# Kernel tuning notes

Hardware: AMD Instinct MI355X
Metric: run time of the kernel (lower is better)

Reference implementation:

```python
import jax, jax.numpy as jnp
import numpy as np

N_NODES = 50000
N_EDGES = 800000
IN_DIM = 256
N_HEADS = 4
D_HEAD = 32  # out_dim // num_heads = 128 // 4
NEG_SLOPE = 0.01  # F.leaky_relu default


def setup_inputs() -> dict:
    key = jax.random.key(0)
    k1, k2, k3, k4, k5 = jax.random.split(key, 5)
    h = jax.random.normal(k1, (N_NODES, IN_DIM), dtype=jnp.float32)
    # per-head projection weights, xavier-ish scale
    fc_w = jax.random.normal(k2, (N_HEADS, IN_DIM, D_HEAD), dtype=jnp.float32) * (1.0 / np.sqrt(IN_DIM))
    attn_w = jax.random.normal(k3, (N_HEADS, 2 * D_HEAD), dtype=jnp.float32) * (1.0 / np.sqrt(2 * D_HEAD))
    src = jax.random.randint(k4, (N_EDGES,), 0, N_NODES, dtype=jnp.int32)
    dst = jax.random.randint(k5, (N_EDGES,), 0, N_NODES, dtype=jnp.int32)
    return {"h": h, "fc_w": fc_w, "attn_w": attn_w, "src": src, "dst": dst,
            "num_bits": 8, "num_grad_bits": 8}


def reference(h, fc_w, attn_w, src, dst, num_bits, num_grad_bits):
    # num_bits/num_grad_bits only used in quant_agg branch (disabled in source)
    N = h.shape[0]
    # per-head linear projection: [N, H, dh]
    z = jnp.einsum('ni,hid->nhd', h, fc_w)
    z_src = z[src]  # [E, H, dh]
    z_dst = z[dst]  # [E, H, dh]
    # edge attention score: attn_fc(cat[z_src, z_dst]) -> split weight halves
    a_src, a_dst = attn_w[:, :D_HEAD], attn_w[:, D_HEAD:]
    e = (jnp.einsum('ehd,hd->eh', z_src, a_src)
         + jnp.einsum('ehd,hd->eh', z_dst, a_dst))  # [E, H]
    e = jnp.where(e >= 0, e, NEG_SLOPE * e)  # leaky_relu
    # segment softmax over incoming edges per destination node
    m = jax.ops.segment_max(e, dst, num_segments=N)  # [N, H]
    ex = jnp.exp(e - m[dst])
    denom = jax.ops.segment_sum(ex, dst, num_segments=N)  # [N, H]
    alpha = ex / denom[dst]  # [E, H]
    # scatter weighted aggregation
    out = jax.ops.segment_sum(alpha[:, :, None] * z_src, dst, num_segments=N)  # [N, H, dh]
    # merge='cat' over heads
    return out.reshape(N, N_HEADS * D_HEAD)
```

## Files before the change

### kernel.cpp

```cpp
#include <hip/hip_runtime.h>
#include <hip/hip_bf16.h>
#include <math.h>

#define N_HEADS 4
#define D_HEAD 32
#define IN_DIM 256
#define OUT_DIM (N_HEADS * D_HEAD)
#define NEG_SLOPE 0.01f

#define BSHIFT 7
#define BUCK_NODES 128
#define CAP 4096
#define CHUNK 8192

typedef __attribute__((ext_vector_type(8))) short bf16x8;
typedef __attribute__((ext_vector_type(4))) float f32x4;
typedef __attribute__((ext_vector_type(2))) float f32x2;

static __device__ __forceinline__ unsigned short f2bf(float x)
{
    unsigned int u = __float_as_uint(x);
    u = u + 0x7FFFu + ((u >> 16) & 1u);
    return (unsigned short)(u >> 16);
}

static __device__ __forceinline__ unsigned int pack_bf2(float a, float b)
{
    union { __hip_bfloat162 b2; unsigned int u; } r;
    r.b2 = __float22bfloat162_rn(make_float2(a, b));
    return r.u;
}

static __device__ __forceinline__ f32x2 bfpair(unsigned int u)
{
    f32x2 r;
    r.x = __uint_as_float(u << 16);
    r.y = __uint_as_float(u & 0xFFFF0000u);
    return r;
}

__global__ void setup_kernel(const float* __restrict__ fc_w,
                             unsigned short* __restrict__ wl,
                             int* __restrict__ bucket_fill, int nbuck)
{
    int o = blockIdx.x * blockDim.x + threadIdx.x;
    if (o < nbuck) bucket_fill[o] = 0;
    if (o >= 32768) return;
    int j  = o & 7;
    int l  = (o >> 3) & 63;
    int kf = (o >> 9) & 7;
    int cf = (o >> 12) & 7;
    int k   = kf * 32 + (l >> 4) * 8 + j;
    int col = cf * 16 + (l & 15);
    int hh = col >> 5, d = col & 31;
    wl[o] = f2bf(fc_w[hh * 8192 + k * 32 + d]);
}

__global__ __launch_bounds__(512, 4) void fused_kernel(
    const float* __restrict__ h, const unsigned short* __restrict__ wl,
    const float* __restrict__ attn_w,
    unsigned int* __restrict__ zb,
    float* __restrict__ s_src, float* __restrict__ s_dst,
    int n_nodes,
    const int* __restrict__ src, const int* __restrict__ dst,
    int* __restrict__ bucket_fill, unsigned int* __restrict__ scratch,
    int n_edges, int nbuck, int nA)
{
    __shared__ __align__(16) char smem[65536];
    const int t = threadIdx.x;

    if (blockIdx.x < nA) {
        int* bhist = (int*)smem;
        int* boff  = (int*)(smem + 2048);
        int* goff  = (int*)(smem + 4096);
        int* bcur  = (int*)(smem + 6144);
        int* stmp  = (int*)(smem + 8192);
        unsigned int* lpair = (unsigned int*)(smem + 10240);

        const int e0 = blockIdx.x * CHUNK;
        const int n  = min(CHUNK, n_edges - e0);

        bhist[t] = 0;
        __syncthreads();

        for (int i = t; i < n; i += 512) {
            atomicAdd(&bhist[dst[e0 + i] >> BSHIFT], 1);
        }
        __syncthreads();

        int v = bhist[t];
        int x = v;
        stmp[t] = x;
        __syncthreads();
        for (int off = 1; off < 512; off <<= 1) {
            int y = (t >= off) ? stmp[t - off] : 0;
            __syncthreads();
            x += y;
            stmp[t] = x;
            __syncthreads();
        }
        int excl = x - v;
        boff[t] = excl;
        bcur[t] = excl;

        goff[t] = (v > 0 && t < nbuck) ? (t * CAP + atomicAdd(&bucket_fill[t], v)) : 0;
        __syncthreads();

        for (int i = t; i < n; i += 512) {
            int d  = dst[e0 + i];
            int sv = src[e0 + i];
            int p  = atomicAdd(&bcur[d >> BSHIFT], 1);
            lpair[p] = ((unsigned int)d << 16) | (unsigned int)sv;
        }
        __syncthreads();

        const int lim = nbuck * CAP - 1;
        for (int i = t; i < n; i += 512) {
            unsigned int u = lpair[i];
            int b = (int)(u >> 16) >> BSHIFT;
            int addr = goff[b] + (i - boff[b]);
            scratch[min(addr, lim)] = u;
        }
        return;
    }

    unsigned short* wls = (unsigned short*)smem;

    #pragma unroll
    for (int it = 0; it < 8; ++it) {
        ((uint4*)wls)[t + it * 512] = ((const uint4*)wl)[t + it * 512];
    }
    __syncthreads();

    const int w  = t >> 6;
    const int l  = t & 63;
    const int g  = l >> 4;
    const int ln = l & 15;
    const int m0 = (blockIdx.x - nA) * 128 + w * 16;

    const int arow = min(m0 + ln, n_nodes - 1);
    const float4* hrow = (const float4*)(h + (size_t)arow * IN_DIM);

    f32x4 acc[8];
    #pragma unroll
    for (int cf = 0; cf < 8; ++cf) acc[cf] = (f32x4){0.f, 0.f, 0.f, 0.f};

    #pragma unroll
    for (int kf = 0; kf < 8; ++kf) {
        float4 alo = hrow[kf * 8 + g * 2];
        float4 ahi = hrow[kf * 8 + g * 2 + 1];
        union { unsigned int u[4]; bf16x8 v; } fa;
        fa.u[0] = pack_bf2(alo.x, alo.y);
        fa.u[1] = pack_bf2(alo.z, alo.w);
        fa.u[2] = pack_bf2(ahi.x, ahi.y);
        fa.u[3] = pack_bf2(ahi.z, ahi.w);

        #pragma unroll
        for (int cf = 0; cf < 8; ++cf) {
            bf16x8 fb = *(const bf16x8*)&wls[((cf * 8 + kf) * 64 + l) * 8];
            acc[cf] = __builtin_amdgcn_mfma_f32_16x16x32_bf16(fa.v, fb, acc[cf], 0, 0, 0);
        }
    }

    float aw_s[8], aw_d[8];
    #pragma unroll
    for (int cf = 0; cf < 8; ++cf) {
        int col = cf * 16 + ln;
        int hh = col >> 5, d = col & 31;
        aw_s[cf] = attn_w[hh * 64 + d];
        aw_d[cf] = attn_w[hh * 64 + 32 + d];
    }

    #pragma unroll
    for (int r = 0; r < 4; ++r) {
        const int row = m0 + 4 * g + r;
        const bool ok = (row < n_nodes);

        float vs0 = acc[0][r] * aw_s[0] + acc[1][r] * aw_s[1];
        float vs1 = acc[2][r] * aw_s[2] + acc[3][r] * aw_s[3];
        float vs2 = acc[4][r] * aw_s[4] + acc[5][r] * aw_s[5];
        float vs3 = acc[6][r] * aw_s[6] + acc[7][r] * aw_s[7];
        float vd0 = acc[0][r] * aw_d[0] + acc[1][r] * aw_d[1];
        float vd1 = acc[2][r] * aw_d[2] + acc[3][r] * aw_d[3];
        float vd2 = acc[4][r] * aw_d[4] + acc[5][r] * aw_d[5];
        float vd3 = acc[6][r] * aw_d[6] + acc[7][r] * aw_d[7];
        #pragma unroll
        for (int mk = 1; mk < 16; mk <<= 1) {
            vs0 += __shfl_xor(vs0, mk); vs1 += __shfl_xor(vs1, mk);
            vs2 += __shfl_xor(vs2, mk); vs3 += __shfl_xor(vs3, mk);
            vd0 += __shfl_xor(vd0, mk); vd1 += __shfl_xor(vd1, mk);
            vd2 += __shfl_xor(vd2, mk); vd3 += __shfl_xor(vd3, mk);
        }
        float sel_s = (ln == 0) ? vs0 : (ln == 1) ? vs1 : (ln == 2) ? vs2 : vs3;
        float sel_d = ((ln & 3) == 0) ? vd0 : ((ln & 3) == 1) ? vd1 : ((ln & 3) == 2) ? vd2 : vd3;
        if (ok && ln < 4)              s_src[row * N_HEADS + ln]       = sel_s;
        if (ok && ln >= 4 && ln < 8)   s_dst[row * N_HEADS + (ln & 3)] = sel_d;

        #pragma unroll
        for (int cf = 0; cf < 8; ++cf) {
            float v = acc[cf][r];
            float o = __shfl_xor(v, 1);
            if (!(ln & 1) && ok) {
                zb[(size_t)row * 64 + cf * 8 + (ln >> 1)] = pack_bf2(v, o);
            }
        }
    }
}

__global__ __launch_bounds__(256) void bucketB_kernel(
    const unsigned int* __restrict__ scratch,
    const int* __restrict__ bucket_fill,
    int* __restrict__ row_start,
    int* __restrict__ sorted_src,
    int n_nodes, int nbuck, int n_edges)
{
    __shared__ int pref[512];
    __shared__ int lhist[128];
    __shared__ int lcur[128];
    __shared__ int stmp[256];
    __shared__ unsigned int ent[CAP];

    const int b = blockIdx.x;
    const int t = threadIdx.x;

    {
        int a0 = (2 * t     < nbuck) ? min(bucket_fill[2 * t],     CAP) : 0;
        int a1 = (2 * t + 1 < nbuck) ? min(bucket_fill[2 * t + 1], CAP) : 0;
        int s = a0 + a1;
        int x = s;
        stmp[t] = x;
        __syncthreads();
        for (int off = 1; off < 256; off <<= 1) {
            int y = (t >= off) ? stmp[t - off] : 0;
            __syncthreads();
            x += y;
            stmp[t] = x;
            __syncthreads();
        }
        int excl = x - s;
        pref[2 * t]     = excl;
        pref[2 * t + 1] = excl + a0;
    }
    __syncthreads();

    const int cnt_b = min(bucket_fill[b], CAP);
    const int row0  = pref[b];
    const unsigned int* sb = scratch + (size_t)b * CAP;

    if (b == 0 && t == 0) row_start[n_nodes] = n_edges;

    if (t < 128) lhist[t] = 0;
    __syncthreads();

    for (int i = t; i < cnt_b; i += 256) {
        unsigned int u = sb[i];
        ent[i] = u;
        atomicAdd(&lhist[(u >> 16) & (BUCK_NODES - 1)], 1);
    }
    __syncthreads();

    int v = (t < 128) ? lhist[t] : 0;
    int x = v;
    stmp[t] = x;
    __syncthreads();
    for (int off = 1; off < 128; off <<= 1) {
        int y = (t >= off) ? stmp[t - off] : 0;
        __syncthreads();
        x += y;
        stmp[t] = x;
        __syncthreads();
    }
    if (t < 128) {
        int excl = x - v;
        lcur[t] = excl;
        int node = b * BUCK_NODES + t;
        if (node < n_nodes) row_start[node] = row0 + excl;
    }
    __syncthreads();

    for (int i = t; i < cnt_b; i += 256) {
        unsigned int u = ent[i];
        int dl = (u >> 16) & (BUCK_NODES - 1);
        int r = atomicAdd(&lcur[dl], 1);
        sorted_src[row0 + r] = (int)(u & 0xFFFFu);
    }
}

__global__ __launch_bounds__(256) void gather_kernel(
    const int* __restrict__ sorted_src, const int* __restrict__ row_start,
    const unsigned int* __restrict__ zb,
    const float* __restrict__ s_src, const float* __restrict__ s_dst,
    float* __restrict__ out, int n_nodes)
{
    int wave = (blockIdx.x * 256 + threadIdx.x) >> 6;
    int lane = threadIdx.x & 63;
    int half = lane >> 5;
    int node = wave * 2 + half;
    int g2   = (lane >> 4) & 1;
    int q    = lane & 15;
    int hh   = q >> 2;

    const bool valid = (node < n_nodes);
    const int nclamp = min(node, n_nodes - 1);
    const int b0 = row_start[nclamp];
    int deg = row_start[nclamp + 1] - b0;
    if (!valid) deg = 0;

    f32x2 acc2[4];
    #pragma unroll
    for (int i = 0; i < 4; ++i) acc2[i] = (f32x2){0.f, 0.f};
    float den = 0.0f;

    if (deg > 0) {
        const int* sp = sorted_src + b0;
        const float sdst = s_dst[nclamp * N_HEADS + hh];
        const int dm1 = deg - 1;

        for (int p = 0; p < deg; p += 8) {
            int i0 = p + g2, i1 = p + 2 + g2, i2 = p + 4 + g2, i3 = p + 6 + g2;
            int s0 = sp[min(i0, dm1)];
            int s1 = sp[min(i1, dm1)];
            int s2 = sp[min(i2, dm1)];
            int s3 = sp[min(i3, dm1)];

            float f0 = s_src[s0 * N_HEADS + hh];
            float f1 = s_src[s1 * N_HEADS + hh];
            float f2 = s_src[s2 * N_HEADS + hh];
            float f3 = s_src[s3 * N_HEADS + hh];
            uint4 u0 = *(const uint4*)&zb[(size_t)s0 * 64 + q * 4];
            uint4 u1 = *(const uint4*)&zb[(size_t)s1 * 64 + q * 4];
            uint4 u2 = *(const uint4*)&zb[(size_t)s2 * 64 + q * 4];
            uint4 u3 = *(const uint4*)&zb[(size_t)s3 * 64 + q * 4];

            float e0 = f0 + sdst; e0 = fmaxf(e0, NEG_SLOPE * e0);
            float e1 = f1 + sdst; e1 = fmaxf(e1, NEG_SLOPE * e1);
            float e2 = f2 + sdst; e2 = fmaxf(e2, NEG_SLOPE * e2);
            float e3 = f3 + sdst; e3 = fmaxf(e3, NEG_SLOPE * e3);
            float x0 = (i0 <= dm1) ? __expf(e0) : 0.0f;
            float x1 = (i1 <= dm1) ? __expf(e1) : 0.0f;
            float x2 = (i2 <= dm1) ? __expf(e2) : 0.0f;
            float x3 = (i3 <= dm1) ? __expf(e3) : 0.0f;
            den += (x0 + x1) + (x2 + x3);

            f32x2 xv;
            xv = (f32x2){x0, x0};
            acc2[0] += xv * bfpair(u0.x);
            acc2[1] += xv * bfpair(u0.y);
            acc2[2] += xv * bfpair(u0.z);
            acc2[3] += xv * bfpair(u0.w);
            xv = (f32x2){x1, x1};
            acc2[0] += xv * bfpair(u1.x);
            acc2[1] += xv * bfpair(u1.y);
            acc2[2] += xv * bfpair(u1.z);
            acc2[3] += xv * bfpair(u1.w);
            xv = (f32x2){x2, x2};
            acc2[0] += xv * bfpair(u2.x);
            acc2[1] += xv * bfpair(u2.y);
            acc2[2] += xv * bfpair(u2.z);
            acc2[3] += xv * bfpair(u2.w);
            xv = (f32x2){x3, x3};
            acc2[0] += xv * bfpair(u3.x);
            acc2[1] += xv * bfpair(u3.y);
            acc2[2] += xv * bfpair(u3.z);
            acc2[3] += xv * bfpair(u3.w);
        }
    }

    #pragma unroll
    for (int i = 0; i < 4; ++i) {
        acc2[i].x += __shfl_xor(acc2[i].x, 16);
        acc2[i].y += __shfl_xor(acc2[i].y, 16);
    }
    den += __shfl_xor(den, 16);

    if (g2 == 0 && valid) {
        float inv = (deg > 0) ? 1.0f / den : 0.0f;
        float4 v0 = make_float4(acc2[0].x * inv, acc2[0].y * inv, acc2[1].x * inv, acc2[1].y * inv);
        float4 v1 = make_float4(acc2[2].x * inv, acc2[2].y * inv, acc2[3].x * inv, acc2[3].y * inv);
        float4* op = (float4*)&out[(size_t)node * OUT_DIM + q * 8];
        op[0] = v0;
        op[1] = v1;
    }
}

extern "C" void kernel_launch(void* const* d_in, const int* in_sizes, int n_in,
                              void* d_out, int out_size, void* d_ws, size_t ws_size,
                              hipStream_t stream)
{
    const float* h      = (const float*)d_in[0];
    const float* fc_w   = (const float*)d_in[1];
    const float* attn_w = (const float*)d_in[2];
    const int*   src    = (const int*)d_in[3];
    const int*   dst    = (const int*)d_in[4];

    const int n_nodes = in_sizes[0] / IN_DIM;
    const int n_edges = in_sizes[3];
    const int nbuck   = (n_nodes + BUCK_NODES - 1) / BUCK_NODES;

    float* out = (float*)d_out;

    char* ws = (char*)d_ws;
    unsigned int* zb      = (unsigned int*)ws;
    float* s_src          = (float*)(zb + (size_t)n_nodes * 64);
    float* s_dst          = s_src + (size_t)n_nodes * N_HEADS;
    int*   row_start      = (int*)(s_dst + (size_t)n_nodes * N_HEADS);
    int*   bucket_fill    = row_start + n_nodes + 16;
    int*   sorted_src     = bucket_fill + nbuck + 17;
    unsigned int* scratch = (unsigned int*)(sorted_src + n_edges + 16);
    unsigned short* wl_g  = (unsigned short*)(scratch + (size_t)nbuck * CAP);

    const int nA = (n_edges + CHUNK - 1) / CHUNK;
    const int nG = (n_nodes + 127) / 128;

    setup_kernel<<<128, 256, 0, stream>>>(fc_w, wl_g, bucket_fill, nbuck);

    fused_kernel<<<nA + nG, 512, 0, stream>>>(
        h, wl_g, attn_w, zb, s_src, s_dst, n_nodes,
        src, dst, bucket_fill, scratch, n_edges, nbuck, nA);

    bucketB_kernel<<<nbuck, 256, 0, stream>>>(
        scratch, bucket_fill, row_start, sorted_src, n_nodes, nbuck, n_edges);

    {
        int waves = (n_nodes + 1) / 2;
        int blocks = (waves * 64 + 255) / 256;
        gather_kernel<<<blocks, 256, 0, stream>>>(
            sorted_src, row_start, zb, s_src, s_dst, out, n_nodes);
    }
}
```

Before: 70.84 us.

## Merge bucket-sort second pass into fused kernel with spin-wait completion counter

Folds the bucketB pass into the fused projection/bucketing kernel as extra trailing blocks. Phase-A blocks bump a global completion counter after a threadfence, and bucket blocks spin until every phase-A block has finished before running the prefix scan and local sort, now with 512 threads. This removes one kernel launch and lets the bucket sort overlap with the projection GEMM blocks. It depends on blocks being scheduled in index order to avoid deadlock, and spinning blocks hold CU slots while they wait.

```diff
diff --git a/kernel.cpp b/kernel.cpp
--- a/kernel.cpp
+++ b/kernel.cpp
@@ -44,7 +44,7 @@
                              int* __restrict__ bucket_fill, int nbuck)
 {
     int o = blockIdx.x * blockDim.x + threadIdx.x;
-    if (o < nbuck) bucket_fill[o] = 0;
+    if (o <= nbuck) bucket_fill[o] = 0;
     if (o >= 32768) return;
     int j  = o & 7;
     int l  = (o >> 3) & 63;
@@ -56,7 +56,7 @@
     wl[o] = f2bf(fc_w[hh * 8192 + k * 32 + d]);
 }
 
-__global__ __launch_bounds__(512, 4) void fused_kernel(
+__global__ __launch_bounds__(512, 4) void mega_kernel(
     const float* __restrict__ h, const unsigned short* __restrict__ wl,
     const float* __restrict__ attn_w,
     unsigned int* __restrict__ zb,
@@ -64,7 +64,8 @@
     int n_nodes,
     const int* __restrict__ src, const int* __restrict__ dst,
     int* __restrict__ bucket_fill, unsigned int* __restrict__ scratch,
-    int n_edges, int nbuck, int nA)
+    int* __restrict__ row_start, int* __restrict__ sorted_src,
+    int n_edges, int nbuck, int nA, int nG)
 {
     __shared__ __align__(16) char smem[65536];
     const int t = threadIdx.x;
@@ -121,168 +122,170 @@
             int addr = goff[b] + (i - boff[b]);
             scratch[min(addr, lim)] = u;
         }
+
+        __syncthreads();
+        __threadfence();
+        if (t == 0) atomicAdd(&bucket_fill[nbuck], 1);
         return;
     }
 
-    unsigned short* wls = (unsigned short*)smem;
-
-    #pragma unroll
-    for (int it = 0; it < 8; ++it) {
-        ((uint4*)wls)[t + it * 512] = ((const uint4*)wl)[t + it * 512];
-    }
-    __syncthreads();
-
-    const int w  = t >> 6;
-    const int l  = t & 63;
-    const int g  = l >> 4;
-    const int ln = l & 15;
-    const int m0 = (blockIdx.x - nA) * 128 + w * 16;
-
-    const int arow = min(m0 + ln, n_nodes - 1);
-    const float4* hrow = (const float4*)(h + (size_t)arow * IN_DIM);
-
-    f32x4 acc[8];
-    #pragma unroll
-    for (int cf = 0; cf < 8; ++cf) acc[cf] = (f32x4){0.f, 0.f, 0.f, 0.f};
-
-    #pragma unroll
-    for (int kf = 0; kf < 8; ++kf) {
-        float4 alo = hrow[kf * 8 + g * 2];
-        float4 ahi = hrow[kf * 8 + g * 2 + 1];
-        union { unsigned int u[4]; bf16x8 v; } fa;
-        fa.u[0] = pack_bf2(alo.x, alo.y);
-        fa.u[1] = pack_bf2(alo.z, alo.w);
-        fa.u[2] = pack_bf2(ahi.x, ahi.y);
-        fa.u[3] = pack_bf2(ahi.z, ahi.w);
-
+    if (blockIdx.x < nA + nG) {
+        unsigned short* wls = (unsigned short*)smem;
+
+        #pragma unroll
+        for (int it = 0; it < 8; ++it) {
+            ((uint4*)wls)[t + it * 512] = ((const uint4*)wl)[t + it * 512];
+        }
+        __syncthreads();
+
+        const int w  = t >> 6;
+        const int l  = t & 63;
+        const int g  = l >> 4;
+        const int ln = l & 15;
+        const int m0 = (blockIdx.x - nA) * 128 + w * 16;
+
+        const int arow = min(m0 + ln, n_nodes - 1);
+        const float4* hrow = (const float4*)(h + (size_t)arow * IN_DIM);
+
+        f32x4 acc[8];
+        #pragma unroll
+        for (int cf = 0; cf < 8; ++cf) acc[cf] = (f32x4){0.f, 0.f, 0.f, 0.f};
+
+        #pragma unroll
+        for (int kf = 0; kf < 8; ++kf) {
+            float4 alo = hrow[kf * 8 + g * 2];
+            float4 ahi = hrow[kf * 8 + g * 2 + 1];
+            union { unsigned int u[4]; bf16x8 v; } fa;
+            fa.u[0] = pack_bf2(alo.x, alo.y);
+            fa.u[1] = pack_bf2(alo.z, alo.w);
+            fa.u[2] = pack_bf2(ahi.x, ahi.y);
+            fa.u[3] = pack_bf2(ahi.z, ahi.w);
+
+            #pragma unroll
+            for (int cf = 0; cf < 8; ++cf) {
+                bf16x8 fb = *(const bf16x8*)&wls[((cf * 8 + kf) * 64 + l) * 8];
+                acc[cf] = __builtin_amdgcn_mfma_f32_16x16x32_bf16(fa.v, fb, acc[cf], 0, 0, 0);
+            }
+        }
+
+        float aw_s[8], aw_d[8];
         #pragma unroll
         for (int cf = 0; cf < 8; ++cf) {
-            bf16x8 fb = *(const bf16x8*)&wls[((cf * 8 + kf) * 64 + l) * 8];
-            acc[cf] = __builtin_amdgcn_mfma_f32_16x16x32_bf16(fa.v, fb, acc[cf], 0, 0, 0);
-        }
-    }
-
-    float aw_s[8], aw_d[8];
-    #pragma unroll
-    for (int cf = 0; cf < 8; ++cf) {
-        int col = cf * 16 + ln;
-        int hh = col >> 5, d = col & 31;
-        aw_s[cf] = attn_w[hh * 64 + d];
-        aw_d[cf] = attn_w[hh * 64 + 32 + d];
-    }
-
-    #pragma unroll
-    for (int r = 0; r < 4; ++r) {
-        const int row = m0 + 4 * g + r;
-        const bool ok = (row < n_nodes);
-
-        float vs0 = acc[0][r] * aw_s[0] + acc[1][r] * aw_s[1];
-        float vs1 = acc[2][r] * aw_s[2] + acc[3][r] * aw_s[3];
-        float vs2 = acc[4][r] * aw_s[4] + acc[5][r] * aw_s[5];
-        float vs3 = acc[6][r] * aw_s[6] + acc[7][r] * aw_s[7];
-        float vd0 = acc[0][r] * aw_d[0] + acc[1][r] * aw_d[1];
-        float vd1 = acc[2][r] * aw_d[2] + acc[3][r] * aw_d[3];
-        float vd2 = acc[4][r] * aw_d[4] + acc[5][r] * aw_d[5];
-        float vd3 = acc[6][r] * aw_d[6] + acc[7][r] * aw_d[7];
+            int col = cf * 16 + ln;
+            int hh = col >> 5, d = col & 31;
+            aw_s[cf] = attn_w[hh * 64 + d];
+            aw_d[cf] = attn_w[hh * 64 + 32 + d];
+        }
+
         #pragma unroll
-        for (int mk = 1; mk < 16; mk <<= 1) {
-            vs0 += __shfl_xor(vs0, mk); vs1 += __shfl_xor(vs1, mk);
-            vs2 += __shfl_xor(vs2, mk); vs3 += __shfl_xor(vs3, mk);
-            vd0 += __shfl_xor(vd0, mk); vd1 += __shfl_xor(vd1, mk);
-            vd2 += __shfl_xor(vd2, mk); vd3 += __shfl_xor(vd3, mk);
-        }
-        float sel_s = (ln == 0) ? vs0 : (ln == 1) ? vs1 : (ln == 2) ? vs2 : vs3;
-        float sel_d = ((ln & 3) == 0) ? vd0 : ((ln & 3) == 1) ? vd1 : ((ln & 3) == 2) ? vd2 : vd3;
-        if (ok && ln < 4)              s_src[row * N_HEADS + ln]       = sel_s;
-        if (ok && ln >= 4 && ln < 8)   s_dst[row * N_HEADS + (ln & 3)] = sel_d;
-
-        #pragma unroll
-        for (int cf = 0; cf < 8; ++cf) {
-            float v = acc[cf][r];
-            float o = __shfl_xor(v, 1);
-            if (!(ln & 1) && ok) {
-                zb[(size_t)row * 64 + cf * 8 + (ln >> 1)] = pack_bf2(v, o);
+        for (int r = 0; r < 4; ++r) {
+            const int row = m0 + 4 * g + r;
+            const bool ok = (row < n_nodes);
+
+            float vs0 = acc[0][r] * aw_s[0] + acc[1][r] * aw_s[1];
+            float vs1 = acc[2][r] * aw_s[2] + acc[3][r] * aw_s[3];
+            float vs2 = acc[4][r] * aw_s[4] + acc[5][r] * aw_s[5];
+            float vs3 = acc[6][r] * aw_s[6] + acc[7][r] * aw_s[7];
+            float vd0 = acc[0][r] * aw_d[0] + acc[1][r] * aw_d[1];
+            float vd1 = acc[2][r] * aw_d[2] + acc[3][r] * aw_d[3];
+            float vd2 = acc[4][r] * aw_d[4] + acc[5][r] * aw_d[5];
+            float vd3 = acc[6][r] * aw_d[6] + acc[7][r] * aw_d[7];
+            #pragma unroll
+            for (int mk = 1; mk < 16; mk <<= 1) {
+                vs0 += __shfl_xor(vs0, mk); vs1 += __shfl_xor(vs1, mk);
+                vs2 += __shfl_xor(vs2, mk); vs3 += __shfl_xor(vs3, mk);
+                vd0 += __shfl_xor(vd0, mk); vd1 += __shfl_xor(vd1, mk);
+                vd2 += __shfl_xor(vd2, mk); vd3 += __shfl_xor(vd3, mk);
             }
-        }
-    }
-}
-
-__global__ __launch_bounds__(256) void bucketB_kernel(
-    const unsigned int* __restrict__ scratch,
-    const int* __restrict__ bucket_fill,
-    int* __restrict__ row_start,
-    int* __restrict__ sorted_src,
-    int n_nodes, int nbuck, int n_edges)
-{
-    __shared__ int pref[512];
-    __shared__ int lhist[128];
-    __shared__ int lcur[128];
-    __shared__ int stmp[256];
-    __shared__ unsigned int ent[CAP];
-
-    const int b = blockIdx.x;
-    const int t = threadIdx.x;
+            float sel_s = (ln == 0) ? vs0 : (ln == 1) ? vs1 : (ln == 2) ? vs2 : vs3;
+            float sel_d = ((ln & 3) == 0) ? vd0 : ((ln & 3) == 1) ? vd1 : ((ln & 3) == 2) ? vd2 : vd3;
+            if (ok && ln < 4)              s_src[row * N_HEADS + ln]       = sel_s;
+            if (ok && ln >= 4 && ln < 8)   s_dst[row * N_HEADS + (ln & 3)] = sel_d;
+
+            #pragma unroll
+            for (int cf = 0; cf < 8; ++cf) {
+                float v = acc[cf][r];
+                float o = __shfl_xor(v, 1);
+                if (!(ln & 1) && ok) {
+                    zb[(size_t)row * 64 + cf * 8 + (ln >> 1)] = pack_bf2(v, o);
+                }
+            }
+        }
+        return;
+    }
 
     {
-        int a0 = (2 * t     < nbuck) ? min(bucket_fill[2 * t],     CAP) : 0;
-        int a1 = (2 * t + 1 < nbuck) ? min(bucket_fill[2 * t + 1], CAP) : 0;
-        int s = a0 + a1;
-        int x = s;
-        stmp[t] = x;
-        __syncthreads();
-        for (int off = 1; off < 256; off <<= 1) {
-            int y = (t >= off) ? stmp[t - off] : 0;
-            __syncthreads();
-            x += y;
+        const int b = blockIdx.x - nA - nG;
+        int* pref  = (int*)smem;
+        int* lhist = (int*)(smem + 2048);
+        int* lcur  = (int*)(smem + 2560);
+        int* stmp  = (int*)(smem + 4096);
+        unsigned int* ent = (unsigned int*)(smem + 8192);
+
+        if (t == 0) {
+            while (atomicAdd(&bucket_fill[nbuck], 0) < nA) {
+                __builtin_amdgcn_s_sleep(2);
+            }
+        }
+        __syncthreads();
+        __threadfence();
+
+        {
+            int v = (t < nbuck) ? min(bucket_fill[t], CAP) : 0;
+            int x = v;
             stmp[t] = x;
             __syncthreads();
-        }
-        int excl = x - s;
-        pref[2 * t]     = excl;
-        pref[2 * t + 1] = excl + a0;
-    }
-    __syncthreads();
-
-    const int cnt_b = min(bucket_fill[b], CAP);
-    const int row0  = pref[b];
-    const unsigned int* sb = scratch + (size_t)b * CAP;
-
-    if (b == 0 && t == 0) row_start[n_nodes] = n_edges;
-
-    if (t < 128) lhist[t] = 0;
-    __syncthreads();
-
-    for (int i = t; i < cnt_b; i += 256) {
-        unsigned int u = sb[i];
-        ent[i] = u;
-        atomicAdd(&lhist[(u >> 16) & (BUCK_NODES - 1)], 1);
-    }
-    __syncthreads();
-
-    int v = (t < 128) ? lhist[t] : 0;
-    int x = v;
-    stmp[t] = x;
-    __syncthreads();
-    for (int off = 1; off < 128; off <<= 1) {
-        int y = (t >= off) ? stmp[t - off] : 0;
-        __syncthreads();
-        x += y;
-        stmp[t] = x;
-        __syncthreads();
-    }
-    if (t < 128) {
-        int excl = x - v;
-        lcur[t] = excl;
-        int node = b * BUCK_NODES + t;
-        if (node < n_nodes) row_start[node] = row0 + excl;
-    }
-    __syncthreads();
-
-    for (int i = t; i < cnt_b; i += 256) {
-        unsigned int u = ent[i];
-        int dl = (u >> 16) & (BUCK_NODES - 1);
-        int r = atomicAdd(&lcur[dl], 1);
-        sorted_src[row0 + r] = (int)(u & 0xFFFFu);
+            for (int off = 1; off < 512; off <<= 1) {
+                int y = (t >= off) ? stmp[t - off] : 0;
+                __syncthreads();
+                x += y;
+                stmp[t] = x;
+                __syncthreads();
+            }
+            pref[t] = x - v;
+        }
+        __syncthreads();
+
+        const int cnt_b = min(bucket_fill[b], CAP);
+        const int row0  = pref[b];
+        const unsigned int* sb = scratch + (size_t)b * CAP;
+
+        if (b == 0 && t == 0) row_start[n_nodes] = n_edges;
+
+        if (t < 128) lhist[t] = 0;
+        __syncthreads();
+
+        for (int i = t; i < cnt_b; i += 512) {
+            unsigned int u = sb[i];
+            ent[i] = u;
+            atomicAdd(&lhist[(u >> 16) & (BUCK_NODES - 1)], 1);
+        }
+        __syncthreads();
+
+        int v = (t < 128) ? lhist[t] : 0;
+        int x = v;
+        if (t < 128) stmp[t] = x;
+        __syncthreads();
+        for (int off = 1; off < 128; off <<= 1) {
+            int y = (t >= off && t < 128) ? stmp[t - off] : 0;
+            __syncthreads();
+            if (t < 128) { x += y; stmp[t] = x; }
+            __syncthreads();
+        }
+        if (t < 128) {
+            int excl = x - v;
+            lcur[t] = excl;
+            int node = b * BUCK_NODES + t;
+            if (node < n_nodes) row_start[node] = row0 + excl;
+        }
+        __syncthreads();
+
+        for (int i = t; i < cnt_b; i += 512) {
+            unsigned int u = ent[i];
+            int dl = (u >> 16) & (BUCK_NODES - 1);
+            int r = atomicAdd(&lcur[dl], 1);
+            sorted_src[row0 + r] = (int)(u & 0xFFFFu);
+        }
     }
 }
 
@@ -414,12 +417,10 @@
 
     setup_kernel<<<128, 256, 0, stream>>>(fc_w, wl_g, bucket_fill, nbuck);
 
-    fused_kernel<<<nA + nG, 512, 0, stream>>>(
+    mega_kernel<<<nA + nG + nbuck, 512, 0, stream>>>(
         h, wl_g, attn_w, zb, s_src, s_dst, n_nodes,
-        src, dst, bucket_fill, scratch, n_edges, nbuck, nA);
-
-    bucketB_kernel<<<nbuck, 256, 0, stream>>>(
-        scratch, bucket_fill, row_start, sorted_src, n_nodes, nbuck, n_edges);
+        src, dst, bucket_fill, scratch, row_start, sorted_src,
+        n_edges, nbuck, nA, nG);
 
     {
         int waves = (n_nodes + 1) / 2;
```

Result: slower. 160.7 us (+126.8%).
